# Kernel tuning notes

Hardware: AMD Instinct MI355X
Metric: run time of the kernel (lower is better)

The kernel has to match this reference:

```python
import jax, jax.numpy as jnp
import numpy as np

N_NODES = 50000

def _gcn_conv(x, W, b, src, dst, num_nodes):
    # PyG GCNConv: linear transform, then D^{-1/2} A_hat D^{-1/2} aggregation (A_hat has self-loops).
    xw = x @ W                                   # [N, out]
    ones = jnp.ones(src.shape[0], dtype=x.dtype)
    deg = jax.ops.segment_sum(ones, dst, num_segments=num_nodes)  # in-degree incl. self loop
    dinv = jnp.where(deg > 0, jax.lax.rsqrt(deg), 0.0)
    norm = dinv[src] * dinv[dst]                 # [E]
    msg = xw[src] * norm[:, None]                # [E, out] gather + scale
    out = jax.ops.segment_sum(msg, dst, num_segments=num_nodes)   # scatter-add
    return out + b

def _add_self_loops(edge_index, num_nodes):
    loop = jnp.arange(num_nodes, dtype=edge_index.dtype)
    src = jnp.concatenate([edge_index[0], loop])
    dst = jnp.concatenate([edge_index[1], loop])
    return src, dst

def setup_inputs() -> dict:
    key = jax.random.key(0)
    k = jax.random.split(key, 6)
    in_dim, hid_dim, out_dim = 256, 128, 64
    n_edges = 800000
    x = jax.random.normal(k[0], (N_NODES, in_dim), dtype=jnp.float32)
    edge_index = jax.random.randint(k[1], (2, n_edges), 0, N_NODES, dtype=jnp.int64)
    W1 = jax.random.normal(k[2], (in_dim, hid_dim), dtype=jnp.float32) / np.sqrt(in_dim)
    b1 = jnp.zeros((hid_dim,), dtype=jnp.float32)
    W2 = jax.random.normal(k[3], (hid_dim, out_dim), dtype=jnp.float32) / np.sqrt(hid_dim)
    b2 = jnp.zeros((out_dim,), dtype=jnp.float32)
    return {"x": x, "edge_index": edge_index, "W1": W1, "b1": b1, "W2": W2, "b2": b2}

def reference(x, edge_index, W1, b1, W2, b2):
    src, dst = _add_self_loops(edge_index, N_NODES)
    h = jnp.tanh(_gcn_conv(x, W1, b1, src, dst, N_NODES))
    out = _gcn_conv(h, W2, b2, src, dst, N_NODES)
    return out
```

## Files before the change

### kernel.cpp

```cpp
#include <hip/hip_runtime.h>

#define INDIM 256
#define HID 128
#define OUTD 64
#define BINSHIFT 8
#define MAXBIN 256

typedef _Float16 f16x8 __attribute__((ext_vector_type(8)));
typedef float    f32x4 __attribute__((ext_vector_type(4)));

__global__ __launch_bounds__(256) void k_hist_setup(const int* __restrict__ dst, int* __restrict__ bin_counts,
                                                    int E,
                                                    const float* __restrict__ W1, const float* __restrict__ W2,
                                                    _Float16* __restrict__ W1t, _Float16* __restrict__ W2t) {
    __shared__ int h[MAXBIN];
    int tid = threadIdx.x;
    h[tid] = 0;
    __syncthreads();
    int base = blockIdx.x * 4096;
#pragma unroll
    for (int i = 0; i < 16; i++) {
        int e = base + i * 256 + tid;
        if (e < E) atomicAdd(&h[dst[e] >> BINSHIFT], 1);
    }
    __syncthreads();
    int v = h[tid];
    if (v) atomicAdd(&bin_counts[tid], v);

    constexpr int NW1 = HID * INDIM;
    constexpr int NW2 = OUTD * HID;
    int id = blockIdx.x * 256 + tid;
    if (id < NW1) {
        int n = id / INDIM, k = id % INDIM;
        W1t[id] = (_Float16)W1[k * HID + n];
    } else if (id < NW1 + NW2) {
        int j = id - NW1;
        int n = j / HID, k = j % HID;
        W2t[j] = (_Float16)W2[k * OUTD + n];
    }
}

struct __align__(16) GemmSh { _Float16 As[128][40]; _Float16 Bs[128][40]; };
struct FillSh { int h[256]; int s[256]; int rb[256]; };
struct CsrSh  { int A[256]; int B[256]; int C[256]; };
union FillU { FillSh f; GemmSh g; };
union CsrU  { CsrSh  c; GemmSh g; };

template <int BN, int K, typename AT, int OCW>
__device__ __forceinline__ void gemm_body(const AT* __restrict__ X, const _Float16* __restrict__ Wt,
                                          const float* __restrict__ dscale,
                                          _Float16* __restrict__ XW, int M, int rb,
                                          _Float16 (*As)[40], _Float16 (*Bs)[40])
{
    constexpr int NT = BN / 16;
    const int tid  = threadIdx.x;
    const int wave = tid >> 6;
    const int lane = tid & 63;
    const int m    = lane & 15;
    const int q    = lane >> 4;

    f32x4 acc[2][NT];
#pragma unroll
    for (int r = 0; r < 2; r++)
#pragma unroll
        for (int t = 0; t < NT; t++) acc[r][t] = (f32x4){0.f, 0.f, 0.f, 0.f};

    for (int kt = 0; kt < K; kt += 32) {
        if (kt) __syncthreads();
        if constexpr (sizeof(AT) == 4) {
#pragma unroll
            for (int i = 0; i < 4; i++) {
                int ch = tid + i * 256;
                int row = ch >> 3, c4 = ch & 7, gr = rb + row;
                float4 v = make_float4(0.f, 0.f, 0.f, 0.f);
                if (gr < M) v = *(const float4*)((const float*)X + (long)gr * K + kt + c4 * 4);
                _Float16* p = &As[row][c4 * 4];
                p[0] = (_Float16)v.x; p[1] = (_Float16)v.y;
                p[2] = (_Float16)v.z; p[3] = (_Float16)v.w;
            }
        } else {
#pragma unroll
            for (int i = 0; i < 2; i++) {
                int ch = tid + i * 256;
                int row = ch >> 2, c8 = ch & 3, gr = rb + row;
                int f0 = kt + c8 * 8;
                uint4 v = make_uint4(0u, 0u, 0u, 0u);
                if (gr < M) v = *(const uint4*)((const _Float16*)X + ((long)(f0 >> 4) * M + gr) * 16 + (f0 & 8));
                *(uint4*)(&As[row][c8 * 8]) = v;
            }
        }
#pragma unroll
        for (int i = 0; i < BN / 64; i++) {
            int ch = tid + i * 256;
            int n = ch >> 2, c8 = ch & 3;
            *(uint4*)(&Bs[n][c8 * 8]) = *(const uint4*)(Wt + (long)n * K + kt + c8 * 8);
        }
        __syncthreads();

        f16x8 a0 = *(const f16x8*)(&As[wave * 32 + m][q * 8]);
        f16x8 a1 = *(const f16x8*)(&As[wave * 32 + 16 + m][q * 8]);
#pragma unroll
        for (int t = 0; t < NT; t++) {
            f16x8 bf = *(const f16x8*)(&Bs[t * 16 + m][q * 8]);
            acc[0][t] = __builtin_amdgcn_mfma_f32_16x16x32_f16(a0, bf, acc[0][t], 0, 0, 0);
            acc[1][t] = __builtin_amdgcn_mfma_f32_16x16x32_f16(a1, bf, acc[1][t], 0, 0, 0);
        }
    }

#pragma unroll
    for (int r2 = 0; r2 < 2; r2++) {
        int row0 = rb + wave * 32 + r2 * 16 + q * 4;
#pragma unroll
        for (int rr = 0; rr < 4; rr++) {
            int row = row0 + rr;
            if (row < M) {
                float sc = dscale ? dscale[row] : 1.f;
#pragma unroll
                for (int t = 0; t < NT; t++) {
                    int col = t * 16 + m;
                    long addr = ((long)(col / OCW) * M + row) * OCW + (col % OCW);
                    XW[addr] = (_Float16)(acc[r2][t][rr] * sc);
                }
            }
        }
    }
}

__device__ __forceinline__ void fill_body(const int* __restrict__ src, const int* __restrict__ dst,
                                          const int* __restrict__ bin_counts, int* __restrict__ bin_cursor,
                                          int* __restrict__ binned, int E, FillSh& sh)
{
    int tid = threadIdx.x;
    sh.h[tid] = 0;
    int v = bin_counts[tid];
    sh.s[tid] = v;
    __syncthreads();
    int base = blockIdx.x * 2048;
    int ep[8], eb[8], rk[8];
#pragma unroll
    for (int i = 0; i < 8; i++) {
        int e = base + i * 256 + tid;
        if (e < E) {
            int s = src[e], d = dst[e];
            ep[i] = (s << 8) | (d & 255);
            eb[i] = d >> BINSHIFT;
            rk[i] = atomicAdd(&sh.h[eb[i]], 1);
        } else {
            eb[i] = -1;
        }
    }
#pragma unroll
    for (int off = 1; off < 256; off <<= 1) {
        int t = (tid >= off) ? sh.s[tid - off] : 0;
        __syncthreads();
        sh.s[tid] += t;
        __syncthreads();
    }
    int c = sh.h[tid];
    if (c) sh.rb[tid] = (sh.s[tid] - v) + atomicAdd(&bin_cursor[tid], c);
    __syncthreads();
#pragma unroll
    for (int i = 0; i < 8; i++) {
        if (eb[i] >= 0) binned[sh.rb[eb[i]] + rk[i]] = ep[i];
    }
}

__device__ __forceinline__ void csr_body(const int* __restrict__ binned, const int* __restrict__ bin_counts,
                                         int* __restrict__ row_start, float* __restrict__ dinv,
                                         int* __restrict__ edge_src, int M, int E, CsrSh& sh)
{
    int b = blockIdx.x, tid = threadIdx.x;
    int v = bin_counts[tid];
    sh.A[tid] = v;
    __syncthreads();
#pragma unroll
    for (int off = 1; off < 256; off <<= 1) {
        int t = (tid >= off) ? sh.A[tid - off] : 0;
        __syncthreads();
        sh.A[tid] += t;
        __syncthreads();
    }
    sh.B[tid] = sh.A[tid] - v;
    __syncthreads();
    int beg = sh.B[b];
    int end = (b + 1 < 256) ? sh.B[b + 1] : E;
    if (b == 0 && tid == 0) row_start[M] = E;

    sh.A[tid] = 0;
    __syncthreads();
    for (int i = beg + tid; i < end; i += 256) {
        atomicAdd(&sh.A[binned[i] & 255], 1);
    }
    __syncthreads();
    int c = sh.A[tid];
    sh.B[tid] = c;
    __syncthreads();
#pragma unroll
    for (int off = 1; off < 256; off <<= 1) {
        int t = (tid >= off) ? sh.B[tid - off] : 0;
        __syncthreads();
        sh.B[tid] += t;
        __syncthreads();
    }
    int start = beg + sh.B[tid] - c;
    int node = (b << BINSHIFT) + tid;
    if (node < M) {
        row_start[node] = start;
        dinv[node] = rsqrtf(1.0f + (float)c);
    }
    sh.C[tid] = start;
    __syncthreads();
    for (int i = beg + tid; i < end; i += 256) {
        int p = binned[i];
        int pos = atomicAdd(&sh.C[p & 255], 1);
        edge_src[pos] = p >> 8;
    }
}

__global__ __launch_bounds__(256) void k_binfill_gemm(
    const int* __restrict__ src, const int* __restrict__ dst,
    const int* __restrict__ bin_counts, int* __restrict__ bin_cursor, int* __restrict__ binned, int E,
    const float* __restrict__ X, const _Float16* __restrict__ W1t, _Float16* __restrict__ XW, int M,
    int nfill, int rbofs)
{
    __shared__ FillU u;
    if ((int)blockIdx.x < nfill)
        fill_body(src, dst, bin_counts, bin_cursor, binned, E, u.f);
    else
        gemm_body<HID, INDIM, float, 16>(X, W1t, nullptr, XW, M, (rbofs + (int)blockIdx.x - nfill) * 128, u.g.As, u.g.Bs);
}

__global__ __launch_bounds__(256) void k_csr_gemm(
    const int* __restrict__ binned, const int* __restrict__ bin_counts,
    int* __restrict__ row_start, float* __restrict__ dinv, int* __restrict__ edge_src, int M, int E,
    const float* __restrict__ X, const _Float16* __restrict__ W1t, _Float16* __restrict__ XW,
    int nbin, int rbofs)
{
    __shared__ CsrU u;
    if ((int)blockIdx.x < nbin)
        csr_body(binned, bin_counts, row_start, dinv, edge_src, M, E, u.c);
    else
        gemm_body<HID, INDIM, float, 16>(X, W1t, nullptr, XW, M, (rbofs + (int)blockIdx.x - nbin) * 128, u.g.As, u.g.Bs);
}

__global__ __launch_bounds__(256) void k_gemm2(const _Float16* __restrict__ X, const _Float16* __restrict__ Wt,
                                               const float* __restrict__ dscale,
                                               _Float16* __restrict__ XW, int M)
{
    __shared__ __align__(16) _Float16 As[128][40];
    __shared__ __align__(16) _Float16 Bs[OUTD][40];
    gemm_body<OUTD, HID, _Float16, 8>(X, Wt, dscale, XW, M, (int)blockIdx.x * 128, As, Bs);
}

__global__ __launch_bounds__(256) void k_agg1(
    const int* __restrict__ row_start, const int* __restrict__ edge_src,
    const _Float16* __restrict__ featc,
    const float* __restrict__ bias,
    const float* __restrict__ dinv,
    _Float16* __restrict__ h16c, int M)
{
    const int ch = blockIdx.x & 7;
    const int n = ((int)blockIdx.x >> 3) * 128 + ((int)threadIdx.x >> 1);
    if (n >= M) return;
    const int q2 = threadIdx.x & 1;
    const _Float16* fb = featc + (long)ch * M * 16 + q2 * 8;
    const int fo = ch * 16 + q2 * 8;

    float di = dinv[n];
    int beg = row_start[n], end = row_start[n + 1];
    f16x8 self = *(const f16x8*)(fb + (long)n * 16);
    float acc[8], acc2[8];
#pragma unroll
    for (int k = 0; k < 8; k++) { acc[k] = di * (float)self[k]; acc2[k] = 0.f; }

    int j = beg;
    for (; j + 7 < end; j += 8) {
        int s0 = edge_src[j],     s1 = edge_src[j + 1];
        int s2 = edge_src[j + 2], s3 = edge_src[j + 3];
        int s4 = edge_src[j + 4], s5 = edge_src[j + 5];
        int s6 = edge_src[j + 6], s7 = edge_src[j + 7];
        float d0 = dinv[s0], d1 = dinv[s1], d2 = dinv[s2], d3 = dinv[s3];
        float d4 = dinv[s4], d5 = dinv[s5], d6 = dinv[s6], d7 = dinv[s7];
        f16x8 v0 = *(const f16x8*)(fb + (long)s0 * 16);
        f16x8 v1 = *(const f16x8*)(fb + (long)s1 * 16);
        f16x8 v2 = *(const f16x8*)(fb + (long)s2 * 16);
        f16x8 v3 = *(const f16x8*)(fb + (long)s3 * 16);
        f16x8 v4 = *(const f16x8*)(fb + (long)s4 * 16);
        f16x8 v5 = *(const f16x8*)(fb + (long)s5 * 16);
        f16x8 v6 = *(const f16x8*)(fb + (long)s6 * 16);
        f16x8 v7 = *(const f16x8*)(fb + (long)s7 * 16);
#pragma unroll
        for (int k = 0; k < 8; k++) {
            acc[k]  = fmaf(d0, (float)v0[k], acc[k]);
            acc2[k] = fmaf(d1, (float)v1[k], acc2[k]);
            acc[k]  = fmaf(d2, (float)v2[k], acc[k]);
            acc2[k] = fmaf(d3, (float)v3[k], acc2[k]);
            acc[k]  = fmaf(d4, (float)v4[k], acc[k]);
            acc2[k] = fmaf(d5, (float)v5[k], acc2[k]);
            acc[k]  = fmaf(d6, (float)v6[k], acc[k]);
            acc2[k] = fmaf(d7, (float)v7[k], acc2[k]);
        }
    }
    for (; j + 3 < end; j += 4) {
        int s0 = edge_src[j],     s1 = edge_src[j + 1];
        int s2 = edge_src[j + 2], s3 = edge_src[j + 3];
        float d0 = dinv[s0], d1 = dinv[s1], d2 = dinv[s2], d3 = dinv[s3];
        f16x8 v0 = *(const f16x8*)(fb + (long)s0 * 16);
        f16x8 v1 = *(const f16x8*)(fb + (long)s1 * 16);
        f16x8 v2 = *(const f16x8*)(fb + (long)s2 * 16);
        f16x8 v3 = *(const f16x8*)(fb + (long)s3 * 16);
#pragma unroll
        for (int k = 0; k < 8; k++) {
            acc[k]  = fmaf(d0, (float)v0[k], acc[k]);
            acc2[k] = fmaf(d1, (float)v1[k], acc2[k]);
            acc[k]  = fmaf(d2, (float)v2[k], acc[k]);
            acc2[k] = fmaf(d3, (float)v3[k], acc2[k]);
        }
    }
    for (; j < end; j++) {
        int s = edge_src[j];
        float d = dinv[s];
        f16x8 v = *(const f16x8*)(fb + (long)s * 16);
#pragma unroll
        for (int k = 0; k < 8; k++) acc[k] = fmaf(d, (float)v[k], acc[k]);
    }

    f16x8 hh;
#pragma unroll
    for (int k = 0; k < 8; k++)
        hh[k] = (_Float16)tanhf(bias[fo + k] + di * (acc[k] + acc2[k]));
    *(f16x8*)(h16c + ((long)ch * M + n) * 16 + q2 * 8) = hh;
}

__global__ __launch_bounds__(256) void k_agg2(
    const int* __restrict__ row_start, const int* __restrict__ edge_src,
    const _Float16* __restrict__ featc,
    const float* __restrict__ bias,
    const float* __restrict__ dinv,
    float* __restrict__ out, int M)
{
    const int ch = blockIdx.x & 7;
    const int n = ((int)blockIdx.x >> 3) * 256 + (int)threadIdx.x;
    if (n >= M) return;
    const _Float16* fb = featc + (long)ch * M * 8;
    const int fo = ch * 8;

    int beg = row_start[n], end = row_start[n + 1];
    f16x8 self = *(const f16x8*)(fb + (long)n * 8);
    float acc[8], acc2[8];
#pragma unroll
    for (int k = 0; k < 8; k++) { acc[k] = (float)self[k]; acc2[k] = 0.f; }

    int j = beg;
    for (; j + 7 < end; j += 8) {
        int s0 = edge_src[j],     s1 = edge_src[j + 1];
        int s2 = edge_src[j + 2], s3 = edge_src[j + 3];
        int s4 = edge_src[j + 4], s5 = edge_src[j + 5];
        int s6 = edge_src[j + 6], s7 = edge_src[j + 7];
        f16x8 v0 = *(const f16x8*)(fb + (long)s0 * 8);
        f16x8 v1 = *(const f16x8*)(fb + (long)s1 * 8);
        f16x8 v2 = *(const f16x8*)(fb + (long)s2 * 8);
        f16x8 v3 = *(const f16x8*)(fb + (long)s3 * 8);
        f16x8 v4 = *(const f16x8*)(fb + (long)s4 * 8);
        f16x8 v5 = *(const f16x8*)(fb + (long)s5 * 8);
        f16x8 v6 = *(const f16x8*)(fb + (long)s6 * 8);
        f16x8 v7 = *(const f16x8*)(fb + (long)s7 * 8);
#pragma unroll
        for (int k = 0; k < 8; k++) {
            acc[k]  += (float)v0[k] + (float)v1[k];
            acc2[k] += (float)v2[k] + (float)v3[k];
            acc[k]  += (float)v4[k] + (float)v5[k];
            acc2[k] += (float)v6[k] + (float)v7[k];
        }
    }
    for (; j + 3 < end; j += 4) {
        int s0 = edge_src[j],     s1 = edge_src[j + 1];
        int s2 = edge_src[j + 2], s3 = edge_src[j + 3];
        f16x8 v0 = *(const f16x8*)(fb + (long)s0 * 8);
        f16x8 v1 = *(const f16x8*)(fb + (long)s1 * 8);
        f16x8 v2 = *(const f16x8*)(fb + (long)s2 * 8);
        f16x8 v3 = *(const f16x8*)(fb + (long)s3 * 8);
#pragma unroll
        for (int k = 0; k < 8; k++) {
            acc[k]  += (float)v0[k] + (float)v1[k];
            acc2[k] += (float)v2[k] + (float)v3[k];
        }
    }
    for (; j < end; j++) {
        int s = edge_src[j];
        f16x8 v = *(const f16x8*)(fb + (long)s * 8);
#pragma unroll
        for (int k = 0; k < 8; k++) acc[k] += (float)v[k];
    }

    float di = dinv[n];
    float r[8];
#pragma unroll
    for (int k = 0; k < 8; k++) r[k] = bias[fo + k] + di * (acc[k] + acc2[k]);
    f32x4 o0 = {r[0], r[1], r[2], r[3]};
    f32x4 o1 = {r[4], r[5], r[6], r[7]};
    float* p = out + (long)n * OUTD + fo;
    __builtin_nontemporal_store(o0, (f32x4*)p);
    __builtin_nontemporal_store(o1, (f32x4*)(p + 4));
}

extern "C" void kernel_launch(void* const* d_in, const int* in_sizes, int n_in,
                              void* d_out, int out_size, void* d_ws, size_t ws_size,
                              hipStream_t stream) {
    const float* x  = (const float*)d_in[0];
    const int*   ei = (const int*)d_in[1];
    const float* W1 = (const float*)d_in[2];
    const float* b1 = (const float*)d_in[3];
    const float* W2 = (const float*)d_in[4];
    const float* b2 = (const float*)d_in[5];
    float* out = (float*)d_out;

    const int M = in_sizes[0] / INDIM;
    const int E = in_sizes[1] / 2;
    const int* srcp = ei;
    const int* dstp = ei + E;

    const int Mp   = (M + 63) & ~63;
    const int NBIN = (M + 255) >> BINSHIFT;

    float*     dinv       = (float*)d_ws;
    int*       row_start  = (int*)(dinv + Mp);
    int*       bin_cursor = row_start + Mp;
    int*       bin_counts = bin_cursor + MAXBIN;
    _Float16*  W1t        = (_Float16*)(bin_counts + MAXBIN);
    _Float16*  W2t        = W1t + HID * INDIM;
    int*       binned     = (int*)(W2t + OUTD * HID);
    int*       edge_src   = binned + E;
    _Float16*  xw16c      = (_Float16*)(edge_src + E);
    _Float16*  h16c       = xw16c + (long)M * HID;
    _Float16*  hw16c      = h16c + (long)M * HID;

    const int NWH = (E + 4095) / 4096;
    const int NWF = (E + 2047) / 2048;
    const int GB  = (M + 127) / 128;
    const int GA  = GB / 3;
    const int GBc = GB - GA;

    hipMemsetAsync(bin_cursor, 0, 2 * MAXBIN * sizeof(int), stream);
    k_hist_setup<<<NWH, 256, 0, stream>>>(dstp, bin_counts, E, W1, W2, W1t, W2t);
    k_binfill_gemm<<<NWF + GA, 256, 0, stream>>>(srcp, dstp, bin_counts, bin_cursor, binned, E,
                                                 x, W1t, xw16c, M, NWF, 0);
    k_csr_gemm<<<NBIN + GBc, 256, 0, stream>>>(binned, bin_counts, row_start, dinv, edge_src, M, E,
                                               x, W1t, xw16c, NBIN, GA);

    k_agg1<<<((M + 127) / 128) * 8, 256, 0, stream>>>(row_start, edge_src, xw16c, b1, dinv, h16c, M);

    k_gemm2<<<GB, 256, 0, stream>>>(h16c, W2t, dinv, hw16c, M);

    k_agg2<<<((M + 255) / 256) * 8, 256, 0, stream>>>(row_start, edge_src, hw16c, b2, dinv, out, M);
}
```

Before: 271.7 us.

## Make aggregation kernels persistent with XCC-affine per-channel work queues

Replaces the grid-per-(channel,node-group) aggregation launches with persistent 2048-block kernels. Each block reads its XCC id from a hardware register and pulls node groups from atomic work queues, starting with the channel matching its XCC. The aim is to keep each feature-channel slab resident in one XCC's L2, so gathers from random sources hit locally instead of being spread across all dies. This adds an atomic and two block barriers per group, and it relies on the hardware register layout for the XCC id.

```diff
diff --git a/kernel.cpp b/kernel.cpp
--- a/kernel.cpp
+++ b/kernel.cpp
@@ -8,6 +8,12 @@
 
 typedef _Float16 f16x8 __attribute__((ext_vector_type(8)));
 typedef float    f32x4 __attribute__((ext_vector_type(4)));
+
+__device__ __forceinline__ int xcc_id() {
+    int x;
+    asm("s_getreg_b32 %0, hwreg(20, 0, 32)" : "=s"(x));
+    return x & 7;
+}
 
 __global__ __launch_bounds__(256) void k_hist_setup(const int* __restrict__ dst, int* __restrict__ bin_counts,
                                                     int E,
@@ -252,15 +258,13 @@
     gemm_body<OUTD, HID, _Float16, 8>(X, Wt, dscale, XW, M, (int)blockIdx.x * 128, As, Bs);
 }
 
-__global__ __launch_bounds__(256) void k_agg1(
+__device__ __forceinline__ void agg1_group(
+    int ch, int g,
     const int* __restrict__ row_start, const int* __restrict__ edge_src,
-    const _Float16* __restrict__ featc,
-    const float* __restrict__ bias,
-    const float* __restrict__ dinv,
-    _Float16* __restrict__ h16c, int M)
-{
-    const int ch = blockIdx.x & 7;
-    const int n = ((int)blockIdx.x >> 3) * 128 + ((int)threadIdx.x >> 1);
+    const _Float16* __restrict__ featc, const float* __restrict__ bias,
+    const float* __restrict__ dinv, _Float16* __restrict__ h16c, int M)
+{
+    const int n = g * 128 + ((int)threadIdx.x >> 1);
     if (n >= M) return;
     const int q2 = threadIdx.x & 1;
     const _Float16* fb = featc + (long)ch * M * 16 + q2 * 8;
@@ -332,15 +336,35 @@
     *(f16x8*)(h16c + ((long)ch * M + n) * 16 + q2 * 8) = hh;
 }
 
-__global__ __launch_bounds__(256) void k_agg2(
+__global__ __launch_bounds__(256) void k_agg1_p(
     const int* __restrict__ row_start, const int* __restrict__ edge_src,
-    const _Float16* __restrict__ featc,
-    const float* __restrict__ bias,
-    const float* __restrict__ dinv,
-    float* __restrict__ out, int M)
-{
-    const int ch = blockIdx.x & 7;
-    const int n = ((int)blockIdx.x >> 3) * 256 + (int)threadIdx.x;
+    const _Float16* __restrict__ featc, const float* __restrict__ bias,
+    const float* __restrict__ dinv, _Float16* __restrict__ h16c,
+    int* __restrict__ wq, int ngroups, int M)
+{
+    __shared__ int gsh;
+    const int xcc = xcc_id();
+#pragma unroll 1
+    for (int p = 0; p < 8; p++) {
+        const int ch = (xcc + p) & 7;
+        while (true) {
+            if (threadIdx.x == 0) gsh = atomicAdd(&wq[ch], 1);
+            __syncthreads();
+            int g = gsh;
+            __syncthreads();
+            if (g >= ngroups) break;
+            agg1_group(ch, g, row_start, edge_src, featc, bias, dinv, h16c, M);
+        }
+    }
+}
+
+__device__ __forceinline__ void agg2_group(
+    int ch, int g,
+    const int* __restrict__ row_start, const int* __restrict__ edge_src,
+    const _Float16* __restrict__ featc, const float* __restrict__ bias,
+    const float* __restrict__ dinv, float* __restrict__ out, int M)
+{
+    const int n = g * 256 + (int)threadIdx.x;
     if (n >= M) return;
     const _Float16* fb = featc + (long)ch * M * 8;
     const int fo = ch * 8;
@@ -404,6 +428,28 @@
     __builtin_nontemporal_store(o1, (f32x4*)(p + 4));
 }
 
+__global__ __launch_bounds__(256) void k_agg2_p(
+    const int* __restrict__ row_start, const int* __restrict__ edge_src,
+    const _Float16* __restrict__ featc, const float* __restrict__ bias,
+    const float* __restrict__ dinv, float* __restrict__ out,
+    int* __restrict__ wq, int ngroups, int M)
+{
+    __shared__ int gsh;
+    const int xcc = xcc_id();
+#pragma unroll 1
+    for (int p = 0; p < 8; p++) {
+        const int ch = (xcc + p) & 7;
+        while (true) {
+            if (threadIdx.x == 0) gsh = atomicAdd(&wq[ch], 1);
+            __syncthreads();
+            int g = gsh;
+            __syncthreads();
+            if (g >= ngroups) break;
+            agg2_group(ch, g, row_start, edge_src, featc, bias, dinv, out, M);
+        }
+    }
+}
+
 extern "C" void kernel_launch(void* const* d_in, const int* in_sizes, int n_in,
                               void* d_out, int out_size, void* d_ws, size_t ws_size,
                               hipStream_t stream) {
@@ -427,7 +473,9 @@
     int*       row_start  = (int*)(dinv + Mp);
     int*       bin_cursor = row_start + Mp;
     int*       bin_counts = bin_cursor + MAXBIN;
-    _Float16*  W1t        = (_Float16*)(bin_counts + MAXBIN);
+    int*       wq1        = bin_counts + MAXBIN;
+    int*       wq2        = wq1 + 8;
+    _Float16*  W1t        = (_Float16*)(wq2 + 8);
     _Float16*  W2t        = W1t + HID * INDIM;
     int*       binned     = (int*)(W2t + OUTD * HID);
     int*       edge_src   = binned + E;
@@ -440,17 +488,19 @@
     const int GB  = (M + 127) / 128;
     const int GA  = GB / 3;
     const int GBc = GB - GA;
-
-    hipMemsetAsync(bin_cursor, 0, 2 * MAXBIN * sizeof(int), stream);
+    const int ngr1 = (M + 127) / 128;
+    const int ngr2 = (M + 255) / 256;
+
+    hipMemsetAsync(bin_cursor, 0, (2 * MAXBIN + 16) * sizeof(int), stream);
     k_hist_setup<<<NWH, 256, 0, stream>>>(dstp, bin_counts, E, W1, W2, W1t, W2t);
     k_binfill_gemm<<<NWF + GA, 256, 0, stream>>>(srcp, dstp, bin_counts, bin_cursor, binned, E,
                                                  x, W1t, xw16c, M, NWF, 0);
     k_csr_gemm<<<NBIN + GBc, 256, 0, stream>>>(binned, bin_counts, row_start, dinv, edge_src, M, E,
                                                x, W1t, xw16c, NBIN, GA);
 
-    k_agg1<<<((M + 127) / 128) * 8, 256, 0, stream>>>(row_start, edge_src, xw16c, b1, dinv, h16c, M);
+    k_agg1_p<<<2048, 256, 0, stream>>>(row_start, edge_src, xw16c, b1, dinv, h16c, wq1, ngr1, M);
 
     k_gemm2<<<GB, 256, 0, stream>>>(h16c, W2t, dinv, hw16c, M);
 
-    k_agg2<<<((M + 255) / 256) * 8, 256, 0, stream>>>(row_start, edge_src, hw16c, b2, dinv, out, M);
-}
+    k_agg2_p<<<2048, 256, 0, stream>>>(row_start, edge_src, hw16c, b2, dinv, out, wq2, ngr2, M);
+}
```

After: 651.1 us. 2.4x slower.
